# Kernel optimization log

Hardware: AMD Instinct MI355X
Metric: run time of the kernel (lower is better)

The kernel has to match this reference:

```python
import jax, jax.numpy as jnp
import numpy as np

BATCH = 4096
IN_SIZES = [1024, 1024, 1024, 1024]
EMB = 2048  # embracement_size


def setup_inputs() -> dict:
    key = jax.random.key(0)
    keys = jax.random.split(key, 3 * len(IN_SIZES))
    inp = {}
    for i, d in enumerate(IN_SIZES):
        inp[f"x{i}"] = jax.random.normal(keys[3 * i], (BATCH, d), dtype=jnp.float32)
        # Linear params (Kaiming-ish scale)
        inp[f"W{i}"] = jax.random.normal(keys[3 * i + 1], (d, EMB), dtype=jnp.float32) / np.sqrt(d)
        inp[f"b{i}"] = jax.random.normal(keys[3 * i + 2], (EMB,), dtype=jnp.float32) * 0.01
    return inp


def _sample_indices(batch, num_feats, emb):
    # availabilities=None, selection_probabilities=None -> uniform p over modalities
    # multinomial(p, num_samples=emb, replacement=True) == categorical over log p
    logits = jnp.zeros((batch, num_feats), dtype=jnp.float32)  # uniform
    k = jax.random.key(42)
    # shape (emb, batch) broadcasts against logits batch shape (batch,)
    idx = jax.random.categorical(k, logits, axis=-1, shape=(emb, batch))
    return idx.T  # [batch, emb]


def reference(x0, W0, b0, x1, W1, b1, x2, W2, b2, x3, W3, b3):
    xs = [x0, x1, x2, x3]
    Ws = [W0, W1, W2, W3]
    bs = [b0, b1, b2, b3]
    # docking: Linear + ReLU per modality -> [batch, EMB, num_feats]
    dock = jnp.stack([jax.nn.relu(x @ W + b) for x, W, b in zip(xs, Ws, bs)], axis=-1)
    B, E, F = dock.shape
    idx = _sample_indices(B, F, E)  # [B, E] int32
    # gather along modality axis (replaces one-hot multiply-sum)
    out = jnp.take_along_axis(dock, idx[:, :, None], axis=-1)[..., 0]
    return out  # [batch, EMB]
```

## Files before the change

kernel.cpp:

```cpp
#include <hip/hip_runtime.h>
#include <stdint.h>


typedef short short8 __attribute__((ext_vector_type(8)));
typedef float floatx4 __attribute__((ext_vector_type(4)));

#define B_DIM 4096
#define K_DIM 1024
#define E_DIM 2048

__device__ __forceinline__ uint16_t f2bf(float x) {
  uint32_t u = __float_as_uint(x);
  u += 0x7FFFu + ((u >> 16) & 1u);
  return (uint16_t)(u >> 16);
}

__device__ __forceinline__ void threefry(uint32_t x0, uint32_t x1,
                                         uint32_t& o0, uint32_t& o1) {
  const uint32_t ks0 = 0u;
  const uint32_t ks1 = 42u;
  const uint32_t ks2 = 0x1BD11BDAu ^ 42u;
  x0 += ks0; x1 += ks1;
#define TF_R(r) { x0 += x1; x1 = (x1 << r) | (x1 >> (32 - r)); x1 ^= x0; }
  TF_R(13) TF_R(15) TF_R(26) TF_R(6)
  x0 += ks1; x1 += ks2 + 1u;
  TF_R(17) TF_R(29) TF_R(16) TF_R(24)
  x0 += ks2; x1 += ks0 + 2u;
  TF_R(13) TF_R(15) TF_R(26) TF_R(6)
  x0 += ks0; x1 += ks1 + 3u;
  TF_R(17) TF_R(29) TF_R(16) TF_R(24)
  x0 += ks1; x1 += ks2 + 4u;
  TF_R(13) TF_R(15) TF_R(26) TF_R(6)
  x0 += ks2; x1 += ks0 + 5u;
#undef TF_R
  o0 = x0; o1 = x1;
}

__global__ __launch_bounds__(256) void idx_kernel(uint32_t* __restrict__ idx2) {
  uint32_t tid = blockIdx.x * 256u + threadIdx.x;
  uint32_t base = tid << 6;
  uint32_t word = 0;
#pragma unroll 4
  for (int j = 0; j < 16; ++j) {
    uint32_t c = base + 4u * j;
    uint32_t best = 0, bi = 0;
#pragma unroll
    for (uint32_t f = 0; f < 4; ++f) {
      uint32_t y0, y1;
      threefry(0u, c + f, y0, y1);
      uint32_t m = (y0 ^ y1) >> 9;
      if (f == 0) best = m;
      else if (m > best) { best = m; bi = f; }
    }
    word |= bi << (2 * j);
  }
  idx2[tid] = word;
}

__global__ __launch_bounds__(256) void convert_all(
    const float* __restrict__ x0, const float* __restrict__ x1,
    const float* __restrict__ x2, const float* __restrict__ x3,
    const float* __restrict__ W0, const float* __restrict__ W1,
    const float* __restrict__ W2, const float* __restrict__ W3,
    uint16_t* __restrict__ xb, uint16_t* __restrict__ Wt) {
  int z = blockIdx.z;
  if (z < 4) {
    const float* x = (z == 0) ? x0 : (z == 1) ? x1 : (z == 2) ? x2 : x3;
    size_t i = ((size_t)blockIdx.x * 256 + threadIdx.x) * 4;
    float4 v = *(const float4*)(x + i);
    union { uint16_t h[4]; uint64_t q; } p;
    p.h[0] = f2bf(v.x); p.h[1] = f2bf(v.y);
    p.h[2] = f2bf(v.z); p.h[3] = f2bf(v.w);
    *(uint64_t*)(xb + (size_t)z * B_DIM * K_DIM + i) = p.q;
  } else {
    if (blockIdx.x >= 2048) return;
    int f = z - 4;
    const float* W = (f == 0) ? W0 : (f == 1) ? W1 : (f == 2) ? W2 : W3;
    __shared__ float tile[32][33];
    int e0 = (blockIdx.x & 63) * 32, k0 = (blockIdx.x >> 6) * 32;
    int tx = threadIdx.x & 31, ty = threadIdx.x >> 5;
#pragma unroll
    for (int i = 0; i < 4; ++i)
      tile[ty + i * 8][tx] = W[(size_t)(k0 + ty + i * 8) * E_DIM + e0 + tx];
    __syncthreads();
    int t = threadIdx.x;
    int el = t >> 3, kc = (t & 7) * 4;
    union { uint16_t h[4]; uint64_t q; } p;
#pragma unroll
    for (int i = 0; i < 4; ++i) p.h[i] = f2bf(tile[kc + i][el]);
    uint16_t* dst = Wt + (size_t)f * E_DIM * K_DIM;
    *(uint64_t*)(dst + (size_t)(e0 + el) * K_DIM + k0 + kc) = p.q;
  }
}

__device__ __forceinline__ void async16(const uint16_t* g, uint16_t* lds) {
  __builtin_amdgcn_global_load_lds(
      (const __attribute__((address_space(1))) void*)g,
      (__attribute__((address_space(3))) void*)lds, 16, 0, 0);
}

__global__ __launch_bounds__(512, 4) void gemm_fused(
    const uint16_t* __restrict__ Ab, const uint16_t* __restrict__ Bbt,
    const uint32_t* __restrict__ idx2,
    const float* __restrict__ bias0, const float* __restrict__ bias1,
    const float* __restrict__ bias2, const float* __restrict__ bias3,
    float* __restrict__ out) {
  __shared__ uint16_t As[2][128 * 32];
  __shared__ uint16_t Bs[2][128 * 32];

  const int tid = threadIdx.x;
  const int w = tid >> 6;
  const int l = tid & 63;
  const int mBase = blockIdx.y * 128;
  const int nBase = blockIdx.x * 128;

  const int wm = (w >> 2) * 64;
  const int wn = (w & 3) * 32;
  const int sr = l >> 2, sc8 = l & 3;
  const int fr = l & 15, fq = l >> 4;

  const int b_hi0 = (mBase + wm) >> 4;
  uint32_t iw[2][4];
#pragma unroll
  for (int ni = 0; ni < 2; ++ni) {
    int col = nBase + wn + ni * 16 + fr;
#pragma unroll
    for (int mi = 0; mi < 4; ++mi)
      iw[ni][mi] = idx2[(size_t)col * (B_DIM / 16) + b_hi0 + mi];
  }

  floatx4 res[4][2] = {};

#pragma unroll 1
  for (int f = 0; f < 4; ++f) {
    const uint16_t* A = Ab  + (size_t)f * B_DIM * K_DIM + (size_t)mBase * K_DIM;
    const uint16_t* B = Bbt + (size_t)f * E_DIM * K_DIM + (size_t)nBase * K_DIM;
    const uint16_t* Aw = A + (size_t)(16 * w + sr) * K_DIM + sc8 * 8;
    const uint16_t* Bw = B + (size_t)(16 * w + sr) * K_DIM + sc8 * 8;

    floatx4 acc[4][2] = {};

    async16(Aw, &As[0][w * 512]);
    async16(Bw, &Bs[0][w * 512]);
    __syncthreads();

    int buf = 0;
#pragma unroll 1
    for (int kt = 0; kt < 32; ++kt) {
      int k0 = kt * 32;
      if (kt + 1 < 32) {
        async16(Aw + k0 + 32, &As[buf ^ 1][w * 512]);
        async16(Bw + k0 + 32, &Bs[buf ^ 1][w * 512]);
      }
      short8 a[4], b[2];
      #pragma unroll
      for (int mi = 0; mi < 4; ++mi)
        a[mi] = *(const short8*)&As[buf][(wm + mi * 16 + fr) * 32 + fq * 8];
      #pragma unroll
      for (int ni = 0; ni < 2; ++ni)
        b[ni] = *(const short8*)&Bs[buf][(wn + ni * 16 + fr) * 32 + fq * 8];
      #pragma unroll
      for (int mi = 0; mi < 4; ++mi)
        #pragma unroll
        for (int ni = 0; ni < 2; ++ni)
          acc[mi][ni] = __builtin_amdgcn_mfma_f32_16x16x32_bf16(
              a[mi], b[ni], acc[mi][ni], 0, 0, 0);
      __syncthreads();
      buf ^= 1;
    }

    const float* bias = (f == 0) ? bias0 : (f == 1) ? bias1
                      : (f == 2) ? bias2 : bias3;
    #pragma unroll
    for (int ni = 0; ni < 2; ++ni) {
      float bvf = bias[nBase + wn + ni * 16 + fr];
      #pragma unroll
      for (int mi = 0; mi < 4; ++mi) {
        uint32_t wd = iw[ni][mi];
        #pragma unroll
        for (int r = 0; r < 4; ++r) {
          uint32_t sel = (wd >> (2 * (fq * 4 + r))) & 3u;
          if (sel == (uint32_t)f) res[mi][ni][r] = acc[mi][ni][r] + bvf;
        }
      }
    }
  }

#pragma unroll
  for (int ni = 0; ni < 2; ++ni) {
    int col = nBase + wn + ni * 16 + fr;
#pragma unroll
    for (int mi = 0; mi < 4; ++mi) {
      int row0 = mBase + wm + mi * 16 + fq * 4;
#pragma unroll
      for (int r = 0; r < 4; ++r) {
        float o = res[mi][ni][r];
        __builtin_nontemporal_store(o > 0.f ? o : 0.f,
                                    &out[(size_t)(row0 + r) * E_DIM + col]);
      }
    }
  }
}

extern "C" void kernel_launch(void* const* d_in, const int* in_sizes, int n_in,
                              void* d_out, int out_size, void* d_ws, size_t ws_size,
                              hipStream_t stream) {
  const float* x[4]; const float* W[4]; const float* bs[4];
  for (int f = 0; f < 4; ++f) {
    x[f]  = (const float*)d_in[3 * f + 0];
    W[f]  = (const float*)d_in[3 * f + 1];
    bs[f] = (const float*)d_in[3 * f + 2];
  }
  char* ws = (char*)d_ws;
  uint16_t* xb  = (uint16_t*)ws;
  uint16_t* Wt  = (uint16_t*)(ws + (size_t)32 * 1024 * 1024);
  uint32_t* idx2 = (uint32_t*)(ws + (size_t)48 * 1024 * 1024);
  float* out = (float*)d_out;

  idx_kernel<<<dim3(2048), dim3(256), 0, stream>>>(idx2);
  convert_all<<<dim3(4096, 1, 8), dim3(256), 0, stream>>>(
      x[0], x[1], x[2], x[3], W[0], W[1], W[2], W[3], xb, Wt);
  gemm_fused<<<dim3(E_DIM / 128, B_DIM / 128), dim3(512), 0, stream>>>(
      xb, Wt, idx2, bs[0], bs[1], bs[2], bs[3], out);
}
```

Before: 306.2 us.

## Merge index and conversion kernels; XOR-swizzle GEMM LDS tiles to cut bank conflicts

```diff
diff --git a/kernel.cpp b/kernel.cpp
--- a/kernel.cpp
+++ b/kernel.cpp
@@ -36,54 +36,58 @@
   o0 = x0; o1 = x1;
 }
 
-__global__ __launch_bounds__(256) void idx_kernel(uint32_t* __restrict__ idx2) {
-  uint32_t tid = blockIdx.x * 256u + threadIdx.x;
-  uint32_t base = tid << 6;
-  uint32_t word = 0;
-#pragma unroll 4
-  for (int j = 0; j < 16; ++j) {
-    uint32_t c = base + 4u * j;
-    uint32_t best = 0, bi = 0;
-#pragma unroll
-    for (uint32_t f = 0; f < 4; ++f) {
-      uint32_t y0, y1;
-      threefry(0u, c + f, y0, y1);
-      uint32_t m = (y0 ^ y1) >> 9;
-      if (f == 0) best = m;
-      else if (m > best) { best = m; bi = f; }
-    }
-    word |= bi << (2 * j);
-  }
-  idx2[tid] = word;
-}
-
-__global__ __launch_bounds__(256) void convert_all(
+__global__ __launch_bounds__(256) void prep_kernel(
     const float* __restrict__ x0, const float* __restrict__ x1,
     const float* __restrict__ x2, const float* __restrict__ x3,
     const float* __restrict__ W0, const float* __restrict__ W1,
     const float* __restrict__ W2, const float* __restrict__ W3,
-    uint16_t* __restrict__ xb, uint16_t* __restrict__ Wt) {
-  int z = blockIdx.z;
-  if (z < 4) {
-    const float* x = (z == 0) ? x0 : (z == 1) ? x1 : (z == 2) ? x2 : x3;
-    size_t i = ((size_t)blockIdx.x * 256 + threadIdx.x) * 4;
+    uint16_t* __restrict__ xb, uint16_t* __restrict__ Wt,
+    uint32_t* __restrict__ idx2) {
+  __shared__ float tile[32][33];
+  const uint32_t g = blockIdx.x;
+  const uint32_t chunk = g / 13u, slot = g % 13u;
+  const int t = threadIdx.x;
+
+  if (slot == 0) {
+    uint32_t tid = chunk * 256u + t;
+    uint32_t base = tid << 6;
+    uint32_t word = 0;
+#pragma unroll 4
+    for (int j = 0; j < 16; ++j) {
+      uint32_t c = base + 4u * j;
+      uint32_t best = 0, bi = 0;
+#pragma unroll
+      for (uint32_t f = 0; f < 4; ++f) {
+        uint32_t y0, y1;
+        threefry(0u, c + f, y0, y1);
+        uint32_t m = (y0 ^ y1) >> 9;
+        if (f == 0) best = m;
+        else if (m > best) { best = m; bi = f; }
+      }
+      word |= bi << (2 * j);
+    }
+    idx2[tid] = word;
+  } else if (slot <= 8) {
+    uint32_t xi = chunk * 8u + (slot - 1);
+    int f = xi >> 12;
+    const float* x = (f == 0) ? x0 : (f == 1) ? x1 : (f == 2) ? x2 : x3;
+    size_t i = ((size_t)(xi & 4095) * 256 + t) * 4;
     float4 v = *(const float4*)(x + i);
     union { uint16_t h[4]; uint64_t q; } p;
     p.h[0] = f2bf(v.x); p.h[1] = f2bf(v.y);
     p.h[2] = f2bf(v.z); p.h[3] = f2bf(v.w);
-    *(uint64_t*)(xb + (size_t)z * B_DIM * K_DIM + i) = p.q;
+    *(uint64_t*)(xb + (size_t)f * B_DIM * K_DIM + i) = p.q;
   } else {
-    if (blockIdx.x >= 2048) return;
-    int f = z - 4;
+    uint32_t wi = chunk * 4u + (slot - 9);
+    int f = wi >> 11;
+    uint32_t ip = wi & 2047;
     const float* W = (f == 0) ? W0 : (f == 1) ? W1 : (f == 2) ? W2 : W3;
-    __shared__ float tile[32][33];
-    int e0 = (blockIdx.x & 63) * 32, k0 = (blockIdx.x >> 6) * 32;
-    int tx = threadIdx.x & 31, ty = threadIdx.x >> 5;
+    int e0 = (ip & 63) * 32, k0 = (ip >> 6) * 32;
+    int tx = t & 31, ty = t >> 5;
 #pragma unroll
     for (int i = 0; i < 4; ++i)
       tile[ty + i * 8][tx] = W[(size_t)(k0 + ty + i * 8) * E_DIM + e0 + tx];
     __syncthreads();
-    int t = threadIdx.x;
     int el = t >> 3, kc = (t & 7) * 4;
     union { uint16_t h[4]; uint64_t q; } p;
 #pragma unroll
@@ -116,8 +120,10 @@
 
   const int wm = (w >> 2) * 64;
   const int wn = (w & 3) * 32;
-  const int sr = l >> 2, sc8 = l & 3;
+  const int sr = l >> 2;
+  const int sc8 = (l & 3) ^ ((l >> 3) & 3);
   const int fr = l & 15, fq = l >> 4;
+  const int fqs = (fq ^ ((fr >> 1) & 3)) * 8;
 
   const int b_hi0 = (mBase + wm) >> 4;
   uint32_t iw[2][4];
@@ -155,10 +161,10 @@
       short8 a[4], b[2];
       #pragma unroll
       for (int mi = 0; mi < 4; ++mi)
-        a[mi] = *(const short8*)&As[buf][(wm + mi * 16 + fr) * 32 + fq * 8];
+        a[mi] = *(const short8*)&As[buf][(wm + mi * 16 + fr) * 32 + fqs];
       #pragma unroll
       for (int ni = 0; ni < 2; ++ni)
-        b[ni] = *(const short8*)&Bs[buf][(wn + ni * 16 + fr) * 32 + fq * 8];
+        b[ni] = *(const short8*)&Bs[buf][(wn + ni * 16 + fr) * 32 + fqs];
       #pragma unroll
       for (int mi = 0; mi < 4; ++mi)
         #pragma unroll
@@ -217,9 +223,8 @@
   uint32_t* idx2 = (uint32_t*)(ws + (size_t)48 * 1024 * 1024);
   float* out = (float*)d_out;
 
-  idx_kernel<<<dim3(2048), dim3(256), 0, stream>>>(idx2);
-  convert_all<<<dim3(4096, 1, 8), dim3(256), 0, stream>>>(
-      x[0], x[1], x[2], x[3], W[0], W[1], W[2], W[3], xb, Wt);
+  prep_kernel<<<dim3(26624), dim3(256), 0, stream>>>(
+      x[0], x[1], x[2], x[3], W[0], W[1], W[2], W[3], xb, Wt, idx2);
   gemm_fused<<<dim3(E_DIM / 128, B_DIM / 128), dim3(512), 0, stream>>>(
       xb, Wt, idx2, bs[0], bs[1], bs[2], bs[3], out);
 }
```

Result: no change. 303.2 us (-1.0%).
